# Optimization experiments

Measured on AMD Instinct MI355X. Metric: run time of the kernel, lower is better.

Reference implementation:

```python
import jax, jax.numpy as jnp
import numpy as np
import math

D_MODEL = 2048
HEADS = 16
D_K = D_MODEL // HEADS
B, S = 4, 2048


def setup_inputs() -> dict:
    key = jax.random.key(0)
    ks = jax.random.split(key, 11)
    scale = 1.0 / math.sqrt(D_MODEL)
    inp = {
        "q": jax.random.normal(ks[0], (B, S, D_MODEL), dtype=jnp.float32),
        "k": jax.random.normal(ks[1], (B, S, D_MODEL), dtype=jnp.float32),
        "v": jax.random.normal(ks[2], (B, S, D_MODEL), dtype=jnp.float32),
        "w_q": jax.random.normal(ks[3], (D_MODEL, D_MODEL), dtype=jnp.float32) * scale,
        "b_q": jnp.zeros((D_MODEL,), dtype=jnp.float32),
        "w_k": jax.random.normal(ks[4], (D_MODEL, D_MODEL), dtype=jnp.float32) * scale,
        "b_k": jnp.zeros((D_MODEL,), dtype=jnp.float32),
        "w_v": jax.random.normal(ks[5], (D_MODEL, D_MODEL), dtype=jnp.float32) * scale,
        "b_v": jnp.zeros((D_MODEL,), dtype=jnp.float32),
        "w_o": jax.random.normal(ks[6], (D_MODEL, D_MODEL), dtype=jnp.float32) * scale,
        "b_o": jnp.zeros((D_MODEL,), dtype=jnp.float32),
    }
    return inp


def reference(q, k, v, w_q, b_q, w_k, b_k, w_v, b_v, w_o, b_o):
    # Linear projections (torch Linear: x @ W^T + b; here W stored pre-transposed)
    query = q @ w_q + b_q  # [B,S,D]
    key = k @ w_k + b_k
    value = v @ w_v + b_v
    # split heads -> [B,H,S,d_k]
    def split(x):
        return x.reshape(B, S, HEADS, D_K).transpose(0, 2, 1, 3)
    qh, kh, vh = split(query), split(key), split(value)
    # scaled dot-product attention (full score matrix, as in original)
    scores = jnp.einsum('bhqd,bhkd->bhqk', qh, kh) / jnp.sqrt(jnp.float32(D_K))
    attn = jax.nn.softmax(scores, axis=-1)
    out = jnp.einsum('bhqk,bhkd->bhqd', attn, vh)  # [B,H,S,d_k]
    out = out.transpose(0, 2, 1, 3).reshape(B, S, D_MODEL)
    return out @ w_o + b_o
```

## Files before the change

### kernel.cpp

```cpp
#include <hip/hip_runtime.h>
#include <hip/hip_bf16.h>

#define DMODEL 2048
#define HEADS 16
#define DK 128
#define BATCH 4
#define SEQ 2048
#define MROWS (BATCH * SEQ)

typedef __attribute__((ext_vector_type(8))) short bf16x8;
typedef __attribute__((ext_vector_type(4))) short bf16x4;
typedef __attribute__((ext_vector_type(4))) float f32x4;
typedef __attribute__((ext_vector_type(16))) float f32x16;

static __device__ __forceinline__ short f2bf(float x) {
    __hip_bfloat16 h = __float2bfloat16(x);
    union { __hip_bfloat16 h; short s; } u;
    u.h = h;
    return u.s;
}

static __device__ __forceinline__ int cvt_pk_bf16(float lo, float hi) {
    int r;
    asm("v_cvt_pk_bf16_f32 %0, %1, %2" : "=v"(r) : "v"(lo), "v"(hi));
    return r;
}

static __device__ __forceinline__ float exp2_fast(float x) {
    float r;
    asm("v_exp_f32 %0, %1" : "=v"(r) : "v"(x));
    return r;
}

#define MFMA16(a, b, c) __builtin_amdgcn_mfma_f32_16x16x32_bf16((a), (b), (c), 0, 0, 0)
#define MFMA32(a, b, c) __builtin_amdgcn_mfma_f32_32x32x16_bf16((a), (b), (c), 0, 0, 0)

static __device__ __forceinline__ void load_lds16(const void* g, void* l) {
    __builtin_amdgcn_global_load_lds(
        (const __attribute__((address_space(1))) unsigned int*)g,
        (__attribute__((address_space(3))) unsigned int*)l, 16, 0, 0);
}

__global__ __launch_bounds__(256) void cvt_bf16(const float* __restrict__ in,
                                                short* __restrict__ out, int n8) {
    int i = blockIdx.x * blockDim.x + threadIdx.x;
    const int stride = gridDim.x * blockDim.x;
    for (; i < n8; i += stride) {
        f32x4 a = ((const f32x4*)in)[i * 2];
        f32x4 b = ((const f32x4*)in)[i * 2 + 1];
        bf16x8 o;
        o[0] = f2bf(a[0]); o[1] = f2bf(a[1]); o[2] = f2bf(a[2]); o[3] = f2bf(a[3]);
        o[4] = f2bf(b[0]); o[5] = f2bf(b[1]); o[6] = f2bf(b[2]); o[7] = f2bf(b[3]);
        ((bf16x8*)out)[i] = o;
    }
}

__global__ __launch_bounds__(256) void cvt_tr(const float* __restrict__ W,
                                              short* __restrict__ Wt) {
    __shared__ short t[64][72];
    const int n0 = blockIdx.x * 64, k0 = blockIdx.y * 64;
    const int tid = threadIdx.x;
#pragma unroll
    for (int p = 0; p < 4; p++) {
        const int kr = p * 16 + (tid >> 4);
        const int nc = (tid & 15) * 4;
        f32x4 v = *(const f32x4*)&W[(size_t)(k0 + kr) * DMODEL + n0 + nc];
#pragma unroll
        for (int j = 0; j < 4; j++) t[nc + j][kr] = f2bf(v[j]);
    }
    __syncthreads();
    const int nr = tid >> 2, ch = (tid & 3) * 16;
    *(bf16x8*)&Wt[(size_t)(n0 + nr) * DMODEL + k0 + ch] = *(const bf16x8*)&t[nr][ch];
    *(bf16x8*)&Wt[(size_t)(n0 + nr) * DMODEL + k0 + ch + 8] = *(const bf16x8*)&t[nr][ch + 8];
}

__global__ __launch_bounds__(256) void tr_bf16(const short* __restrict__ in,
                                               short* __restrict__ out) {
    __shared__ short t[64][65];
    const int c0 = blockIdx.x * 64, r0 = blockIdx.y * 64;
    const int tid = threadIdx.x;
    const int row = tid >> 2, cb = (tid & 3) * 16;
    bf16x8 a = *(const bf16x8*)&in[(size_t)(r0 + row) * DMODEL + c0 + cb];
    bf16x8 b2 = *(const bf16x8*)&in[(size_t)(r0 + row) * DMODEL + c0 + cb + 8];
#pragma unroll
    for (int j = 0; j < 8; j++) { t[cb + j][row] = a[j]; t[cb + 8 + j][row] = b2[j]; }
    __syncthreads();
#pragma unroll
    for (int j = 0; j < 16; j++)
        out[(size_t)(c0 + row) * MROWS + r0 + cb + j] = t[row][cb + j];
}

static __device__ __forceinline__ void stage2(const char* gbase, char* lbase,
                                              int rb, int r8, int scol, int ktb) {
#pragma unroll
    for (int i = 0; i < 2; i++)
        load_lds16(gbase + (size_t)(rb + i * 8 + r8) * (DMODEL * 2) + ktb + scol,
                   lbase + (rb + i * 8) * 128);
}

template <typename OT, bool TRANSV = false>
__global__ __launch_bounds__(512, 2) void gemm8(
    const short* __restrict__ A, const short* __restrict__ Bt,
    const float* __restrict__ bias, OT* __restrict__ C, float oscale) {
    __shared__ short Asl[256 * 64];
    __shared__ short Bsl[256 * 64];
    const int tid = threadIdx.x, lane = tid & 63, wid = tid >> 6;

    const int nwg = gridDim.x;
    const int bid = blockIdx.x;
    const int swz = (bid & 7) * (nwg >> 3) + (bid >> 3);
    const int bx = swz >> 5, by = swz & 31;
    const int row0 = by * 256, col0 = bx * 256;
    const int wm = wid >> 2, wn = wid & 3;

    const int r8 = lane >> 3;
    const int scol = ((lane & 7) * 16) ^ (r8 << 4);
    const int a1r = ((wid & 4) << 5) + (wid & 3) * 16;
    const int b1r = (wid >> 1) * 64 + (wid & 1) * 16;

    const char* Ab = (const char*)A + (size_t)row0 * (DMODEL * 2);
    const char* Bb = (const char*)Bt + (size_t)col0 * (DMODEL * 2);

    const int arow = wm * 128 + (lane & 15);
    const int brow = wn * 64 + (lane & 15);
    const int fg = (lane >> 4) * 16;
    const int fx = (lane & 7) << 4;

    f32x4 acc[8][4] = {};
    bf16x8 af[4][2], bfr[4][2];

    const int NT = DMODEL / 64;

    stage2(Ab, (char*)Asl, a1r, r8, scol, 0);
    stage2(Bb, (char*)Bsl, b1r, r8, scol, 0);
    stage2(Bb, (char*)Bsl, b1r + 32, r8, scol, 0);
    stage2(Ab, (char*)Asl, a1r + 64, r8, scol, 0);

    for (int t = 0; t < NT; t++) {
        const bool more = (t + 1) < NT;
        const int ktb = (t + 1) * 128;

        asm volatile("s_waitcnt vmcnt(4)" ::: "memory");
        asm volatile("s_waitcnt lgkmcnt(0)" ::: "memory");
        __builtin_amdgcn_s_barrier();
        __builtin_amdgcn_sched_barrier(0);
#pragma unroll
        for (int m = 0; m < 4; m++)
#pragma unroll
            for (int kk = 0; kk < 2; kk++)
                af[m][kk] = *(const bf16x8*)((const char*)Asl + (arow + m * 16) * 128 + ((kk * 64 + fg) ^ fx));
#pragma unroll
        for (int n = 0; n < 2; n++)
#pragma unroll
            for (int kk = 0; kk < 2; kk++)
                bfr[n][kk] = *(const bf16x8*)((const char*)Bsl + (brow + n * 16) * 128 + ((kk * 64 + fg) ^ fx));
        __builtin_amdgcn_s_setprio(1);
#pragma unroll
        for (int m = 0; m < 4; m++)
#pragma unroll
            for (int n = 0; n < 2; n++)
#pragma unroll
                for (int kk = 0; kk < 2; kk++)
                    acc[m][n] = MFMA16(af[m][kk], bfr[n][kk], acc[m][n]);
        __builtin_amdgcn_s_setprio(0);

        asm volatile("s_waitcnt vmcnt(2)" ::: "memory");
        asm volatile("s_waitcnt lgkmcnt(0)" ::: "memory");
        __builtin_amdgcn_s_barrier();
        __builtin_amdgcn_sched_barrier(0);
#pragma unroll
        for (int n = 2; n < 4; n++)
#pragma unroll
            for (int kk = 0; kk < 2; kk++)
                bfr[n][kk] = *(const bf16x8*)((const char*)Bsl + (brow + n * 16) * 128 + ((kk * 64 + fg) ^ fx));
        if (more) {
            stage2(Ab, (char*)Asl, a1r, r8, scol, ktb);
            stage2(Bb, (char*)Bsl, b1r, r8, scol, ktb);
        }
        __builtin_amdgcn_s_setprio(1);
#pragma unroll
        for (int m = 0; m < 4; m++)
#pragma unroll
            for (int n = 2; n < 4; n++)
#pragma unroll
                for (int kk = 0; kk < 2; kk++)
                    acc[m][n] = MFMA16(af[m][kk], bfr[n][kk], acc[m][n]);
        __builtin_amdgcn_s_setprio(0);

        if (more) asm volatile("s_waitcnt vmcnt(4)" ::: "memory");
        else      asm volatile("s_waitcnt vmcnt(0)" ::: "memory");
        asm volatile("s_waitcnt lgkmcnt(0)" ::: "memory");
        __builtin_amdgcn_s_barrier();
        __builtin_amdgcn_sched_barrier(0);
#pragma unroll
        for (int mi = 0; mi < 4; mi++)
#pragma unroll
            for (int kk = 0; kk < 2; kk++)
                af[mi][kk] = *(const bf16x8*)((const char*)Asl + (arow + 64 + mi * 16) * 128 + ((kk * 64 + fg) ^ fx));
        if (more) stage2(Bb, (char*)Bsl, b1r + 32, r8, scol, ktb);
        __builtin_amdgcn_s_setprio(1);
#pragma unroll
        for (int mi = 0; mi < 4; mi++)
#pragma unroll
            for (int n = 2; n < 4; n++)
#pragma unroll
                for (int kk = 0; kk < 2; kk++)
                    acc[4 + mi][n] = MFMA16(af[mi][kk], bfr[n][kk], acc[4 + mi][n]);
        __builtin_amdgcn_s_setprio(0);

        asm volatile("s_waitcnt lgkmcnt(0)" ::: "memory");
        __builtin_amdgcn_s_barrier();
        __builtin_amdgcn_sched_barrier(0);
        if (more) stage2(Ab, (char*)Asl, a1r + 64, r8, scol, ktb);
        __builtin_amdgcn_s_setprio(1);
#pragma unroll
        for (int mi = 0; mi < 4; mi++)
#pragma unroll
            for (int n = 0; n < 2; n++)
#pragma unroll
                for (int kk = 0; kk < 2; kk++)
                    acc[4 + mi][n] = MFMA16(af[mi][kk], bfr[n][kk], acc[4 + mi][n]);
        __builtin_amdgcn_s_setprio(0);
    }

#pragma unroll
    for (int n = 0; n < 4; n++) {
        const int col = col0 + wn * 64 + n * 16 + (lane & 15);
        const float bz = bias[col];
#pragma unroll
        for (int m = 0; m < 8; m++) {
            const int row4 = row0 + wm * 128 + m * 16 + (lane >> 4) * 4;
            if constexpr (TRANSV) {
                bf16x4 tv;
#pragma unroll
                for (int j = 0; j < 4; j++) tv[j] = f2bf((acc[m][n][j] + bz) * oscale);
                *(bf16x4*)&C[(size_t)col * MROWS + row4] = tv;
            } else {
#pragma unroll
                for (int j = 0; j < 4; j++) {
                    const float v = (acc[m][n][j] + bz) * oscale;
                    if constexpr (sizeof(OT) == 2)
                        C[(size_t)(row4 + j) * DMODEL + col] = (OT)f2bf(v);
                    else
                        C[(size_t)(row4 + j) * DMODEL + col] = (OT)v;
                }
            }
        }
    }
}

template <typename AT, typename OT>
__global__ __launch_bounds__(256) void gemm_kernel(
    const AT* __restrict__ A, const float* __restrict__ W,
    const float* __restrict__ bias, OT* __restrict__ C, float oscale) {
    const int K = DMODEL, N = DMODEL;
    __shared__ short As[128][40];
    __shared__ short Bs[128][40];
    const int tid = threadIdx.x;
    const int lane = tid & 63;
    const int wid = tid >> 6;
    const int wm = wid >> 1, wn = wid & 1;
    const int row0 = blockIdx.y * 128;
    const int col0 = blockIdx.x * 128;
    f32x4 acc[4][4] = {};
    const int a_row = tid >> 1;
    const int a_col = (tid & 1) * 16;
    const int b_n = (tid & 31) * 4;
    const int b_k = (tid >> 5) * 4;
    for (int k0 = 0; k0 < K; k0 += 32) {
        __syncthreads();
        {
            const AT* src = A + (size_t)(row0 + a_row) * K + k0 + a_col;
            if constexpr (sizeof(AT) == 4) {
                const float* sf = reinterpret_cast<const float*>(src);
                f32x4 v0 = *(const f32x4*)(sf + 0);
                f32x4 v1 = *(const f32x4*)(sf + 4);
                f32x4 v2 = *(const f32x4*)(sf + 8);
                f32x4 v3 = *(const f32x4*)(sf + 12);
                bf16x8 w0, w1;
                w0[0] = f2bf(v0[0]); w0[1] = f2bf(v0[1]); w0[2] = f2bf(v0[2]); w0[3] = f2bf(v0[3]);
                w0[4] = f2bf(v1[0]); w0[5] = f2bf(v1[1]); w0[6] = f2bf(v1[2]); w0[7] = f2bf(v1[3]);
                w1[0] = f2bf(v2[0]); w1[1] = f2bf(v2[1]); w1[2] = f2bf(v2[2]); w1[3] = f2bf(v2[3]);
                w1[4] = f2bf(v3[0]); w1[5] = f2bf(v3[1]); w1[6] = f2bf(v3[2]); w1[7] = f2bf(v3[3]);
                *(bf16x8*)&As[a_row][a_col + 0] = w0;
                *(bf16x8*)&As[a_row][a_col + 8] = w1;
            } else {
                const short* ss = reinterpret_cast<const short*>(src);
                *(bf16x8*)&As[a_row][a_col + 0] = *(const bf16x8*)(ss + 0);
                *(bf16x8*)&As[a_row][a_col + 8] = *(const bf16x8*)(ss + 8);
            }
        }
        {
            const float* w0p = W + (size_t)(k0 + b_k + 0) * N + col0 + b_n;
            f32x4 r0 = *(const f32x4*)(w0p);
            f32x4 r1 = *(const f32x4*)(w0p + N);
            f32x4 r2 = *(const f32x4*)(w0p + 2 * N);
            f32x4 r3 = *(const f32x4*)(w0p + 3 * N);
#pragma unroll
            for (int j = 0; j < 4; j++) {
                bf16x4 t;
                t[0] = f2bf(r0[j]); t[1] = f2bf(r1[j]); t[2] = f2bf(r2[j]); t[3] = f2bf(r3[j]);
                *(bf16x4*)&Bs[b_n + j][b_k] = t;
            }
        }
        __syncthreads();
        bf16x8 af[4], bfr[4];
#pragma unroll
        for (int m = 0; m < 4; m++)
            af[m] = *(const bf16x8*)&As[wm * 64 + m * 16 + (lane & 15)][(lane >> 4) * 8];
#pragma unroll
        for (int n = 0; n < 4; n++)
            bfr[n] = *(const bf16x8*)&Bs[wn * 64 + n * 16 + (lane & 15)][(lane >> 4) * 8];
#pragma unroll
        for (int m = 0; m < 4; m++)
#pragma unroll
            for (int n = 0; n < 4; n++)
                acc[m][n] = MFMA16(af[m], bfr[n], acc[m][n]);
    }
#pragma unroll
    for (int m = 0; m < 4; m++) {
#pragma unroll
        for (int n = 0; n < 4; n++) {
            const int col = col0 + wn * 64 + n * 16 + (lane & 15);
            const float bz = bias[col];
#pragma unroll
            for (int j = 0; j < 4; j++) {
                const int row = row0 + wm * 64 + m * 16 + (lane >> 4) * 4 + j;
                const float v = (acc[m][n][j] + bz) * oscale;
                if constexpr (sizeof(OT) == 2)
                    C[(size_t)row * N + col] = (OT)f2bf(v);
                else
                    C[(size_t)row * N + col] = (OT)v;
            }
        }
    }
}

__global__ __launch_bounds__(512) void attn_kernel(
    const short* __restrict__ Qp, const short* __restrict__ Kp,
    const short* __restrict__ Vtp, short* __restrict__ Oout) {
    const int nwg = gridDim.x;
    const int bid = blockIdx.x;
    const int bx = (bid & 7) * (nwg >> 3) + (bid >> 3);
    const int qt = bx & 7;
    const int h = (bx >> 3) & 15;
    const int b = bx >> 7;

    __shared__ short Ks[2][64 * 128];
    __shared__ short Vts[2][128 * 64];

    const int tid = threadIdx.x;
    const int lane = tid & 63;
    const int wid = tid >> 6;
    const int lo = lane & 31;
    const int hi1 = lane >> 5;

    bf16x8 qf[8];
    {
        const short* qrow = Qp + (size_t)(b * SEQ + qt * 256 + wid * 32 + lo) * DMODEL + h * DK;
#pragma unroll
        for (int dk = 0; dk < 8; dk++)
            qf[dk] = *(const bf16x8*)(qrow + dk * 16 + hi1 * 8);
    }

    f32x16 oacc[4] = {};
    float lsum = 0.f;

    const char* Kbase = (const char*)(Kp + (size_t)(b * SEQ) * DMODEL + h * DK);
    const char* Vtbase = (const char*)(Vtp + (size_t)(h * DK) * MROWS + b * SEQ);

    const int cpr = (lane & 15) * 16;
    const int krr = wid * 8 + (lane >> 4);
    const int vdd = wid * 16 + (lane >> 3);
    const int vcp = (lane & 7) * 16;
    const int NT = SEQ / 64;
    const float C12 = 17.3123404906676f;

#pragma unroll
    for (int i = 0; i < 2; i++) {
        const int rr = krr + i * 4;
        load_lds16(Kbase + (size_t)rr * (DMODEL * 2) + (cpr ^ ((rr & 15) << 4)),
                   (char*)Ks[0] + wid * 2048 + i * 1024);
    }
#pragma unroll
    for (int i = 0; i < 2; i++) {
        const int d = vdd + i * 8;
        load_lds16(Vtbase + (size_t)d * (MROWS * 2) + (vcp ^ ((d & 7) << 4)),
                   (char*)Vts[0] + wid * 2048 + i * 1024);
    }
    asm volatile("s_waitcnt vmcnt(0)" ::: "memory");
    __builtin_amdgcn_s_barrier();
    __builtin_amdgcn_sched_barrier(0);

    for (int kt = 0; kt < NT; kt++) {
        const int cur = kt & 1;
        const bool more = (kt + 1) < NT;

        if (more) {
#pragma unroll
            for (int i = 0; i < 2; i++) {
                const int rr = krr + i * 4;
                load_lds16(Kbase + (size_t)((kt + 1) * 64 + rr) * (DMODEL * 2) + (cpr ^ ((rr & 15) << 4)),
                           (char*)Ks[cur ^ 1] + wid * 2048 + i * 1024);
            }
#pragma unroll
            for (int i = 0; i < 2; i++) {
                const int d = vdd + i * 8;
                load_lds16(Vtbase + (size_t)d * (MROWS * 2) + (kt + 1) * 128 + (vcp ^ ((d & 7) << 4)),
                           (char*)Vts[cur ^ 1] + wid * 2048 + i * 1024);
            }
        }

        f32x16 sc[2] = {};
        __builtin_amdgcn_s_setprio(1);
#pragma unroll
        for (int dk = 0; dk < 8; dk++) {
#pragma unroll
            for (int kg = 0; kg < 2; kg++) {
                const int r = kg * 32 + lo;
                const int cb = (dk * 32 + hi1 * 16) ^ ((r & 15) << 4);
                bf16x8 kf = *(const bf16x8*)((char*)Ks[cur] + r * 256 + cb);
                sc[kg] = MFMA32(kf, qf[dk], sc[kg]);
            }
        }
        __builtin_amdgcn_s_setprio(0);

#pragma unroll
        for (int kg = 0; kg < 2; kg++)
#pragma unroll
            for (int r = 0; r < 16; r++)
                sc[kg][r] = exp2_fast(sc[kg][r] - C12);

        {
            float s0 = 0.f, s1 = 0.f, s2 = 0.f, s3 = 0.f;
#pragma unroll
            for (int kg = 0; kg < 2; kg++)
#pragma unroll
                for (int r = 0; r < 16; r += 4) {
                    s0 += sc[kg][r]; s1 += sc[kg][r + 1];
                    s2 += sc[kg][r + 2]; s3 += sc[kg][r + 3];
                }
            lsum += (s0 + s1) + (s2 + s3);
        }

        bf16x8 pa[4];
#pragma unroll
        for (int ks = 0; ks < 4; ks++) {
            const int kg = ks >> 1, hf = ks & 1;
            const int X0 = cvt_pk_bf16(sc[kg][8 * hf + 0], sc[kg][8 * hf + 1]);
            const int X1 = cvt_pk_bf16(sc[kg][8 * hf + 2], sc[kg][8 * hf + 3]);
            const int X2 = cvt_pk_bf16(sc[kg][8 * hf + 4], sc[kg][8 * hf + 5]);
            const int X3 = cvt_pk_bf16(sc[kg][8 * hf + 6], sc[kg][8 * hf + 7]);
            const int L0 = hi1 ? X2 : X0, L1 = hi1 ? X3 : X1;
            const int S0 = hi1 ? X0 : X2, S1 = hi1 ? X1 : X3;
            const int R0 = __shfl_xor(S0, 32, 64);
            const int R1 = __shfl_xor(S1, 32, 64);
            union { int i[4]; bf16x8 v; } u;
            u.i[0] = hi1 ? R0 : L0;
            u.i[1] = hi1 ? R1 : L1;
            u.i[2] = hi1 ? L0 : R0;
            u.i[3] = hi1 ? L1 : R1;
            pa[ks] = u.v;
        }

        __builtin_amdgcn_s_setprio(1);
#pragma unroll
        for (int ks = 0; ks < 4; ks++) {
#pragma unroll
            for (int n = 0; n < 4; n++) {
                const int d = n * 32 + lo;
                const int cb = (ks * 32 + hi1 * 16) ^ ((d & 7) << 4);
                bf16x8 vf = *(const bf16x8*)((char*)Vts[cur] + d * 128 + cb);
                oacc[n] = MFMA32(vf, pa[ks], oacc[n]);
            }
        }
        __builtin_amdgcn_s_setprio(0);

        if (more) {
            asm volatile("s_waitcnt vmcnt(0)" ::: "memory");
            asm volatile("s_waitcnt lgkmcnt(0)" ::: "memory");
            __builtin_amdgcn_s_barrier();
            __builtin_amdgcn_sched_barrier(0);
        }
    }

    const float l = lsum + __shfl_xor(lsum, 32, 64);
    const float inv = 1.0f / l;
    short* obase = Oout + (size_t)(b * SEQ + qt * 256 + wid * 32 + lo) * DMODEL + h * DK;
#pragma unroll
    for (int n = 0; n < 4; n++) {
#pragma unroll
        for (int rr = 0; rr < 8; rr++) {
            const int d = n * 32 + 2 * (rr & 1) + 8 * (rr >> 1) + 4 * hi1;
            const int pkv = cvt_pk_bf16(oacc[n][2 * rr] * inv, oacc[n][2 * rr + 1] * inv);
            *(int*)(obase + d) = pkv;
        }
    }
}

extern "C" void kernel_launch(void* const* d_in, const int* in_sizes, int n_in,
                              void* d_out, int out_size, void* d_ws, size_t ws_size,
                              hipStream_t stream) {
    const float* q   = (const float*)d_in[0];
    const float* k   = (const float*)d_in[1];
    const float* v   = (const float*)d_in[2];
    const float* w_q = (const float*)d_in[3];
    const float* b_q = (const float*)d_in[4];
    const float* w_k = (const float*)d_in[5];
    const float* b_k = (const float*)d_in[6];
    const float* w_v = (const float*)d_in[7];
    const float* b_v = (const float*)d_in[8];
    const float* w_o = (const float*)d_in[9];
    const float* b_o = (const float*)d_in[10];
    float* out = (float*)d_out;

    const size_t PROJ = (size_t)MROWS * DMODEL;
    const size_t WSZ = (size_t)DMODEL * DMODEL;
    const float qscale = 0.08838834764831845f * 1.4426950408889634f;
    const int attn_grid = BATCH * HEADS * (SEQ / 256);

    if (ws_size >= (6 * PROJ + 4 * WSZ) * sizeof(short)) {
        short* qbf = (short*)d_ws;
        short* kbf = qbf + PROJ;
        short* vbf = kbf + PROJ;
        short* Qp  = vbf + PROJ;
        short* Kp  = Qp + PROJ;
        short* Vt  = Kp + PROJ;
        short* wtq = Vt + PROJ;
        short* wtk = wtq + WSZ;
        short* wtv = wtk + WSZ;
        short* wto = wtv + WSZ;
        short* Ao  = qbf;

        const int n8 = (int)(PROJ / 8);
        cvt_bf16<<<2048, 256, 0, stream>>>(q, qbf, n8);
        cvt_bf16<<<2048, 256, 0, stream>>>(k, kbf, n8);
        cvt_bf16<<<2048, 256, 0, stream>>>(v, vbf, n8);
        dim3 gtr(DMODEL / 64, DMODEL / 64);
        cvt_tr<<<gtr, 256, 0, stream>>>(w_q, wtq);
        cvt_tr<<<gtr, 256, 0, stream>>>(w_k, wtk);
        cvt_tr<<<gtr, 256, 0, stream>>>(w_v, wtv);
        cvt_tr<<<gtr, 256, 0, stream>>>(w_o, wto);

        const int nwg8 = (MROWS / 256) * (DMODEL / 256);
        gemm8<short><<<nwg8, 512, 0, stream>>>(qbf, wtq, b_q, Qp, qscale);
        gemm8<short><<<nwg8, 512, 0, stream>>>(kbf, wtk, b_k, Kp, 1.0f);
        gemm8<short, true><<<nwg8, 512, 0, stream>>>(vbf, wtv, b_v, Vt, 1.0f);

        attn_kernel<<<attn_grid, 512, 0, stream>>>(Qp, Kp, Vt, Ao);

        gemm8<float><<<nwg8, 512, 0, stream>>>(Ao, wto, b_o, out, 1.0f);
    } else {
        short* Qp = (short*)d_ws;
        short* Kp = Qp + PROJ;
        short* Vp = Kp + PROJ;
        short* Vt = Vp + PROJ;
        short* Ao = Vt + PROJ;
        dim3 gblk(DMODEL / 128, MROWS / 128);
        gemm_kernel<float, short><<<gblk, 256, 0, stream>>>(q, w_q, b_q, Qp, qscale);
        gemm_kernel<float, short><<<gblk, 256, 0, stream>>>(k, w_k, b_k, Kp, 1.0f);
        gemm_kernel<float, short><<<gblk, 256, 0, stream>>>(v, w_v, b_v, Vp, 1.0f);
        dim3 gtrv(DMODEL / 64, MROWS / 64);
        tr_bf16<<<gtrv, 256, 0, stream>>>(Vp, Vt);
        attn_kernel<<<attn_grid, 512, 0, stream>>>(Qp, Kp, Vt, Ao);
        gemm_kernel<short, float><<<gblk, 256, 0, stream>>>(Ao, w_o, b_o, out, 1.0f);
    }
}
```

Before: 569.7 us.

## Widen attention KV tiles to 128 and overlap QK MFMA with softmax; batch conversion launches

The attention kernel now stages 128-key K and V^T tiles per iteration instead of 64, which halves the number of barriers and loop iterations. It also software-pipelines the QK^T MFMAs for the next 32-key group against the exp2/sum/pack work of the current group. The launch bound gains a minimum-blocks hint of 2. The three activation fp32->bf16 conversions are merged into one kernel, and the four weight transpose-conversions into another, to cut launch count. The cost is doubled LDS use (128 KB per block), which may limit occupancy on each CU, and more register pressure from pa[8].

```diff
diff --git a/kernel.cpp b/kernel.cpp
--- a/kernel.cpp
+++ b/kernel.cpp
@@ -41,23 +41,35 @@
         (__attribute__((address_space(3))) unsigned int*)l, 16, 0, 0);
 }
 
-__global__ __launch_bounds__(256) void cvt_bf16(const float* __restrict__ in,
-                                                short* __restrict__ out, int n8) {
+__global__ __launch_bounds__(256) void cvt3_bf16(
+    const float* __restrict__ i0, const float* __restrict__ i1,
+    const float* __restrict__ i2, short* __restrict__ o0,
+    short* __restrict__ o1, short* __restrict__ o2, int n8) {
     int i = blockIdx.x * blockDim.x + threadIdx.x;
     const int stride = gridDim.x * blockDim.x;
-    for (; i < n8; i += stride) {
-        f32x4 a = ((const f32x4*)in)[i * 2];
-        f32x4 b = ((const f32x4*)in)[i * 2 + 1];
+    for (; i < 3 * n8; i += stride) {
+        const int which = i / n8;
+        const int idx = i - which * n8;
+        const float* in = which == 0 ? i0 : (which == 1 ? i1 : i2);
+        short* out = which == 0 ? o0 : (which == 1 ? o1 : o2);
+        f32x4 a = ((const f32x4*)in)[idx * 2];
+        f32x4 b = ((const f32x4*)in)[idx * 2 + 1];
         bf16x8 o;
         o[0] = f2bf(a[0]); o[1] = f2bf(a[1]); o[2] = f2bf(a[2]); o[3] = f2bf(a[3]);
         o[4] = f2bf(b[0]); o[5] = f2bf(b[1]); o[6] = f2bf(b[2]); o[7] = f2bf(b[3]);
-        ((bf16x8*)out)[i] = o;
-    }
-}
-
-__global__ __launch_bounds__(256) void cvt_tr(const float* __restrict__ W,
-                                              short* __restrict__ Wt) {
+        ((bf16x8*)out)[idx] = o;
+    }
+}
+
+__global__ __launch_bounds__(256) void cvt_tr4(
+    const float* __restrict__ w0, const float* __restrict__ w1,
+    const float* __restrict__ w2, const float* __restrict__ w3,
+    short* __restrict__ t0, short* __restrict__ t1,
+    short* __restrict__ t2, short* __restrict__ t3) {
     __shared__ short t[64][72];
+    const int which = blockIdx.z;
+    const float* W = which == 0 ? w0 : (which == 1 ? w1 : (which == 2 ? w2 : w3));
+    short* Wt = which == 0 ? t0 : (which == 1 ? t1 : (which == 2 ? t2 : t3));
     const int n0 = blockIdx.x * 64, k0 = blockIdx.y * 64;
     const int tid = threadIdx.x;
 #pragma unroll
@@ -336,7 +348,7 @@
     }
 }
 
-__global__ __launch_bounds__(512) void attn_kernel(
+__global__ __launch_bounds__(512, 2) void attn_kernel(
     const short* __restrict__ Qp, const short* __restrict__ Kp,
     const short* __restrict__ Vtp, short* __restrict__ Oout) {
     const int nwg = gridDim.x;
@@ -346,8 +358,8 @@
     const int h = (bx >> 3) & 15;
     const int b = bx >> 7;
 
-    __shared__ short Ks[2][64 * 128];
-    __shared__ short Vts[2][128 * 64];
+    __shared__ short Ks[2][128 * 128];
+    __shared__ short Vts[2][128 * 128];
 
     const int tid = threadIdx.x;
     const int lane = tid & 63;
@@ -369,24 +381,22 @@
     const char* Kbase = (const char*)(Kp + (size_t)(b * SEQ) * DMODEL + h * DK);
     const char* Vtbase = (const char*)(Vtp + (size_t)(h * DK) * MROWS + b * SEQ);
 
-    const int cpr = (lane & 15) * 16;
-    const int krr = wid * 8 + (lane >> 4);
-    const int vdd = wid * 16 + (lane >> 3);
-    const int vcp = (lane & 7) * 16;
-    const int NT = SEQ / 64;
+    const int srow = wid * 16 + (lane >> 4);
+    const int scp = (lane & 15) * 16;
+    const int NT = SEQ / 128;
     const float C12 = 17.3123404906676f;
 
 #pragma unroll
-    for (int i = 0; i < 2; i++) {
-        const int rr = krr + i * 4;
-        load_lds16(Kbase + (size_t)rr * (DMODEL * 2) + (cpr ^ ((rr & 15) << 4)),
-                   (char*)Ks[0] + wid * 2048 + i * 1024);
-    }
-#pragma unroll
-    for (int i = 0; i < 2; i++) {
-        const int d = vdd + i * 8;
-        load_lds16(Vtbase + (size_t)d * (MROWS * 2) + (vcp ^ ((d & 7) << 4)),
-                   (char*)Vts[0] + wid * 2048 + i * 1024);
+    for (int i = 0; i < 4; i++) {
+        const int rr = srow + i * 4;
+        load_lds16(Kbase + (size_t)rr * (DMODEL * 2) + (scp ^ ((rr & 15) << 4)),
+                   (char*)Ks[0] + wid * 4096 + i * 1024);
+    }
+#pragma unroll
+    for (int i = 0; i < 4; i++) {
+        const int dd = srow + i * 4;
+        load_lds16(Vtbase + (size_t)dd * (MROWS * 2) + (scp ^ ((dd & 15) << 4)),
+                   (char*)Vts[0] + wid * 4096 + i * 1024);
     }
     asm volatile("s_waitcnt vmcnt(0)" ::: "memory");
     __builtin_amdgcn_s_barrier();
@@ -398,79 +408,86 @@
 
         if (more) {
 #pragma unroll
-            for (int i = 0; i < 2; i++) {
-                const int rr = krr + i * 4;
-                load_lds16(Kbase + (size_t)((kt + 1) * 64 + rr) * (DMODEL * 2) + (cpr ^ ((rr & 15) << 4)),
-                           (char*)Ks[cur ^ 1] + wid * 2048 + i * 1024);
-            }
-#pragma unroll
-            for (int i = 0; i < 2; i++) {
-                const int d = vdd + i * 8;
-                load_lds16(Vtbase + (size_t)d * (MROWS * 2) + (kt + 1) * 128 + (vcp ^ ((d & 7) << 4)),
-                           (char*)Vts[cur ^ 1] + wid * 2048 + i * 1024);
-            }
-        }
-
-        f32x16 sc[2] = {};
+            for (int i = 0; i < 4; i++) {
+                const int rr = srow + i * 4;
+                load_lds16(Kbase + (size_t)((kt + 1) * 128 + rr) * (DMODEL * 2) + (scp ^ ((rr & 15) << 4)),
+                           (char*)Ks[cur ^ 1] + wid * 4096 + i * 1024);
+            }
+#pragma unroll
+            for (int i = 0; i < 4; i++) {
+                const int dd = srow + i * 4;
+                load_lds16(Vtbase + (size_t)dd * (MROWS * 2) + (kt + 1) * 256 + (scp ^ ((dd & 15) << 4)),
+                           (char*)Vts[cur ^ 1] + wid * 4096 + i * 1024);
+            }
+        }
+
+        f32x16 sc[2];
+        bf16x8 pa[8];
+
+        sc[0] = (f32x16){};
         __builtin_amdgcn_s_setprio(1);
 #pragma unroll
         for (int dk = 0; dk < 8; dk++) {
-#pragma unroll
-            for (int kg = 0; kg < 2; kg++) {
-                const int r = kg * 32 + lo;
-                const int cb = (dk * 32 + hi1 * 16) ^ ((r & 15) << 4);
-                bf16x8 kf = *(const bf16x8*)((char*)Ks[cur] + r * 256 + cb);
-                sc[kg] = MFMA32(kf, qf[dk], sc[kg]);
-            }
+            const int r = 0 * 32 + lo;
+            const int cb = (dk * 32 + hi1 * 16) ^ ((r & 15) << 4);
+            bf16x8 kf = *(const bf16x8*)((char*)Ks[cur] + r * 256 + cb);
+            sc[0] = MFMA32(kf, qf[dk], sc[0]);
         }
         __builtin_amdgcn_s_setprio(0);
 
 #pragma unroll
-        for (int kg = 0; kg < 2; kg++)
-#pragma unroll
-            for (int r = 0; r < 16; r++)
-                sc[kg][r] = exp2_fast(sc[kg][r] - C12);
-
-        {
-            float s0 = 0.f, s1 = 0.f, s2 = 0.f, s3 = 0.f;
-#pragma unroll
-            for (int kg = 0; kg < 2; kg++)
+        for (int g = 0; g < 4; g++) {
+            if (g < 3) {
+                sc[(g + 1) & 1] = (f32x16){};
+                __builtin_amdgcn_s_setprio(1);
+#pragma unroll
+                for (int dk = 0; dk < 8; dk++) {
+                    const int r = (g + 1) * 32 + lo;
+                    const int cb = (dk * 32 + hi1 * 16) ^ ((r & 15) << 4);
+                    bf16x8 kf = *(const bf16x8*)((char*)Ks[cur] + r * 256 + cb);
+                    sc[(g + 1) & 1] = MFMA32(kf, qf[dk], sc[(g + 1) & 1]);
+                }
+                __builtin_amdgcn_s_setprio(0);
+            }
+            {
+                f32x16& s = sc[g & 1];
+#pragma unroll
+                for (int r = 0; r < 16; r++)
+                    s[r] = exp2_fast(s[r] - C12);
+                float s0 = 0.f, s1 = 0.f, s2 = 0.f, s3 = 0.f;
 #pragma unroll
                 for (int r = 0; r < 16; r += 4) {
-                    s0 += sc[kg][r]; s1 += sc[kg][r + 1];
-                    s2 += sc[kg][r + 2]; s3 += sc[kg][r + 3];
+                    s0 += s[r]; s1 += s[r + 1]; s2 += s[r + 2]; s3 += s[r + 3];
                 }
-            lsum += (s0 + s1) + (s2 + s3);
-        }
-
-        bf16x8 pa[4];
-#pragma unroll
-        for (int ks = 0; ks < 4; ks++) {
-            const int kg = ks >> 1, hf = ks & 1;
-            const int X0 = cvt_pk_bf16(sc[kg][8 * hf + 0], sc[kg][8 * hf + 1]);
-            const int X1 = cvt_pk_bf16(sc[kg][8 * hf + 2], sc[kg][8 * hf + 3]);
-            const int X2 = cvt_pk_bf16(sc[kg][8 * hf + 4], sc[kg][8 * hf + 5]);
-            const int X3 = cvt_pk_bf16(sc[kg][8 * hf + 6], sc[kg][8 * hf + 7]);
-            const int L0 = hi1 ? X2 : X0, L1 = hi1 ? X3 : X1;
-            const int S0 = hi1 ? X0 : X2, S1 = hi1 ? X1 : X3;
-            const int R0 = __shfl_xor(S0, 32, 64);
-            const int R1 = __shfl_xor(S1, 32, 64);
-            union { int i[4]; bf16x8 v; } u;
-            u.i[0] = hi1 ? R0 : L0;
-            u.i[1] = hi1 ? R1 : L1;
-            u.i[2] = hi1 ? L0 : R0;
-            u.i[3] = hi1 ? L1 : R1;
-            pa[ks] = u.v;
+                lsum += (s0 + s1) + (s2 + s3);
+#pragma unroll
+                for (int hf = 0; hf < 2; hf++) {
+                    const int X0 = cvt_pk_bf16(s[8 * hf + 0], s[8 * hf + 1]);
+                    const int X1 = cvt_pk_bf16(s[8 * hf + 2], s[8 * hf + 3]);
+                    const int X2 = cvt_pk_bf16(s[8 * hf + 4], s[8 * hf + 5]);
+                    const int X3 = cvt_pk_bf16(s[8 * hf + 6], s[8 * hf + 7]);
+                    const int L0 = hi1 ? X2 : X0, L1 = hi1 ? X3 : X1;
+                    const int S0 = hi1 ? X0 : X2, S1 = hi1 ? X1 : X3;
+                    const int R0 = __shfl_xor(S0, 32, 64);
+                    const int R1 = __shfl_xor(S1, 32, 64);
+                    union { int i[4]; bf16x8 v; } u;
+                    u.i[0] = hi1 ? R0 : L0;
+                    u.i[1] = hi1 ? R1 : L1;
+                    u.i[2] = hi1 ? L0 : R0;
+                    u.i[3] = hi1 ? L1 : R1;
+                    pa[2 * g + hf] = u.v;
+                }
+            }
         }
 
         __builtin_amdgcn_s_setprio(1);
 #pragma unroll
-        for (int ks = 0; ks < 4; ks++) {
+        for (int ks = 0; ks < 8; ks++) {
 #pragma unroll
             for (int n = 0; n < 4; n++) {
                 const int d = n * 32 + lo;
-                const int cb = (ks * 32 + hi1 * 16) ^ ((d & 7) << 4);
-                bf16x8 vf = *(const bf16x8*)((char*)Vts[cur] + d * 128 + cb);
+                const int cb = (ks * 32 + hi1 * 16) ^ ((d & 15) << 4);
+                bf16x8 vf = *(const bf16x8*)((char*)Vts[cur] + d * 256 + cb);
                 oacc[n] = MFMA32(vf, pa[ks], oacc[n]);
             }
         }
@@ -533,14 +550,9 @@
         short* Ao  = qbf;
 
         const int n8 = (int)(PROJ / 8);
-        cvt_bf16<<<2048, 256, 0, stream>>>(q, qbf, n8);
-        cvt_bf16<<<2048, 256, 0, stream>>>(k, kbf, n8);
-        cvt_bf16<<<2048, 256, 0, stream>>>(v, vbf, n8);
-        dim3 gtr(DMODEL / 64, DMODEL / 64);
-        cvt_tr<<<gtr, 256, 0, stream>>>(w_q, wtq);
-        cvt_tr<<<gtr, 256, 0, stream>>>(w_k, wtk);
-        cvt_tr<<<gtr, 256, 0, stream>>>(w_v, wtv);
-        cvt_tr<<<gtr, 256, 0, stream>>>(w_o, wto);
+        cvt3_bf16<<<3072, 256, 0, stream>>>(q, k, v, qbf, kbf, vbf, n8);
+        dim3 gtr(DMODEL / 64, DMODEL / 64, 4);
+        cvt_tr4<<<gtr, 256, 0, stream>>>(w_q, w_k, w_v, w_o, wtq, wtk, wtv, wto);
 
         const int nwg8 = (MROWS / 256) * (DMODEL / 256);
         gemm8<short><<<nwg8, 512, 0, stream>>>(qbf, wtq, b_q, Qp, qscale);
```

After: 543.6 us. 4.6% less time.
